# Kernel optimization log

Hardware: AMD Instinct MI355X
Metric: run time of the kernel (lower is better)

The kernel has to match this reference:

```python
import jax, jax.numpy as jnp
import numpy as np

N_MESH, N_GRID, N_EDGES, D, H = 40962, 200000, 600000, 128, 128


def layer_norm(x, g, b, eps=1e-5):
    mu = x.mean(-1, keepdims=True)
    xc = x - mu
    var = (xc * xc).mean(-1, keepdims=True)
    return xc * jax.lax.rsqrt(var + eps) * g + b


def setup_inputs() -> dict:
    key = jax.random.key(0)
    ks = jax.random.split(key, 16)
    s = 1.0 / np.sqrt(D).astype(np.float32)
    s2 = 1.0 / np.sqrt(2 * D).astype(np.float32)
    return {
        "m2g_efeat": jax.random.normal(ks[0], (N_EDGES, D), jnp.float32),
        "grid_nfeat": jax.random.normal(ks[1], (N_GRID, D), jnp.float32),
        "mesh_nfeat": jax.random.normal(ks[2], (N_MESH, D), jnp.float32),
        "src_idx": jax.random.randint(ks[3], (N_EDGES,), 0, N_MESH, jnp.int32),
        "dst_idx": jnp.sort(jax.random.randint(ks[4], (N_EDGES,), 0, N_GRID, jnp.int32)),
        # edge TMLP (first linear split across efeat/src/dst -- equals Linear on concat)
        "We": jax.random.normal(ks[5], (D, H), jnp.float32) * s,
        "Ws": jax.random.normal(ks[6], (D, H), jnp.float32) * s,
        "Wd": jax.random.normal(ks[7], (D, H), jnp.float32) * s,
        "b0": jnp.zeros((H,), jnp.float32),
        "W1e": jax.random.normal(ks[8], (H, D), jnp.float32) * s,
        "b1e": jnp.zeros((D,), jnp.float32),
        "ge": jnp.ones((D,), jnp.float32),
        "be": jnp.zeros((D,), jnp.float32),
        # node MLP: input = concat(grid_nfeat, aggregated_efeat) -> 2D
        "Wn0": jax.random.normal(ks[9], (2 * D, H), jnp.float32) * s2,
        "bn0": jnp.zeros((H,), jnp.float32),
        "Wn1": jax.random.normal(ks[10], (H, D), jnp.float32) * s,
        "bn1": jnp.zeros((D,), jnp.float32),
        "gn": jnp.ones((D,), jnp.float32),
        "bn": jnp.zeros((D,), jnp.float32),
    }


def reference(m2g_efeat, grid_nfeat, mesh_nfeat, src_idx, dst_idx,
              We, Ws, Wd, b0, W1e, b1e, ge, be,
              Wn0, bn0, Wn1, bn1, gn, bn):
    # edge TMLP: project each input tensor then gather (CUGO truncated-MLP form)
    h = jax.nn.silu(m2g_efeat @ We
                    + (mesh_nfeat @ Ws)[src_idx]
                    + (grid_nfeat @ Wd)[dst_idx]
                    + b0)                                  # [E, H]
    efeat = layer_norm(h @ W1e + b1e, ge, be)              # [E, D]
    # sum aggregation edge->node, then concat with dst node features
    agg = jax.ops.segment_sum(efeat, dst_idx, num_segments=grid_nfeat.shape[0])  # [N_grid, D]
    cat = jnp.concatenate([grid_nfeat, agg], axis=-1)      # [N_grid, 2D]
    hn = jax.nn.silu(cat @ Wn0 + bn0)                      # [N_grid, H]
    dst = layer_norm(hn @ Wn1 + bn1, gn, bn) + grid_nfeat  # residual
    return dst
```

## Files before the change

### kernel.cpp

```cpp
#include <hip/hip_runtime.h>
#include <math.h>

#define NM 40962
#define NG 200000
#define NE 600000

typedef unsigned short u16;
typedef unsigned int u32;
typedef __attribute__((ext_vector_type(8))) short short8;
typedef __attribute__((ext_vector_type(4))) float f32x4;

#define OFF_WE 0
#define OFF_WS 16384
#define OFF_WD 32768
#define OFF_W1 49152
#define OFF_W0 65536
#define OFF_WN1 98304
__device__ u16 g_wp[114688];

__device__ __forceinline__ u32 f2bf(float f) {
  u32 u = __float_as_uint(f);
  return (u + 0x7FFFu + ((u >> 16) & 1u)) >> 16;
}
__device__ __forceinline__ float bfl(u32 h) { return __uint_as_float(h << 16); }
__device__ __forceinline__ float bsel(u32 w, int hiHalf) {
  return hiHalf ? __uint_as_float(w & 0xFFFF0000u) : __uint_as_float(w << 16);
}
__device__ __forceinline__ float silu_f(float x) { return x / (1.f + __expf(-x)); }

#define MFMA16(a, b, c) __builtin_amdgcn_mfma_f32_16x16x32_bf16(a, b, c, 0, 0, 0)

__device__ __forceinline__ void pk_hl(const float* __restrict__ f, short8& hi, short8& lo) {
#pragma unroll
  for (int j = 0; j < 8; ++j) {
    u32 h = f2bf(f[j]);
    hi[j] = (short)h;
    lo[j] = (short)f2bf(f[j] - bfl(h));
  }
}

__device__ __forceinline__ void afrag_hl(const float* __restrict__ X, int row, int k0,
                                         short8& hi, short8& lo) {
  const float4* p = (const float4*)(X + (size_t)row * 128 + k0);
  float4 a = p[0], b = p[1];
  float f[8] = {a.x, a.y, a.z, a.w, b.x, b.y, b.z, b.w};
  pk_hl(f, hi, lo);
}

template <int K>
__device__ __forceinline__ short8 bfrag(const u16* __restrict__ Wp, int n, int k0) {
  return *(const short8*)(Wp + (size_t)n * K + k0);
}

__global__ void prep_kernel(const float* __restrict__ W, int off, int kbits, int total) {
  int K = 1 << kbits;
  for (int i = blockIdx.x * blockDim.x + threadIdx.x; i < total;
       i += gridDim.x * blockDim.x) {
    int n = i >> kbits, k = i & (K - 1);
    g_wp[off + i] = (u16)f2bf(W[(size_t)k * 128 + n]);
  }
}

__global__ __launch_bounds__(256) void proj_kernel(const float* __restrict__ X,
                                                   int woff, uint4* __restrict__ O,
                                                   int nrows) {
  const u16* Wp = g_wp + woff;
  const int lane = threadIdx.x & 63, wv = threadIdx.x >> 6;
  const int g = lane >> 4, c = lane & 15;
  const int nw = gridDim.x * 4;
  for (int t = blockIdx.x * 4 + wv; t * 32 < nrows; t += nw) {
    const int n0 = t * 32;
    f32x4 acc[2][8];
#pragma unroll
    for (int mt = 0; mt < 2; ++mt)
#pragma unroll
      for (int nt = 0; nt < 8; ++nt) {
        f32x4 z = {0.f, 0.f, 0.f, 0.f};
        acc[mt][nt] = z;
      }
#pragma unroll
    for (int kt = 0; kt < 4; ++kt) {
      short8 ah[2], al[2];
#pragma unroll
      for (int mt = 0; mt < 2; ++mt) {
        int row = n0 + 16 * mt + c;
        if (row >= nrows) row = nrows - 1;
        afrag_hl(X, row, 32 * kt + 8 * g, ah[mt], al[mt]);
      }
#pragma unroll
      for (int nt = 0; nt < 8; ++nt) {
        short8 b = bfrag<128>(Wp, 16 * nt + c, 32 * kt + 8 * g);
#pragma unroll
        for (int mt = 0; mt < 2; ++mt) {
          acc[mt][nt] = MFMA16(ah[mt], b, acc[mt][nt]);
          acc[mt][nt] = MFMA16(al[mt], b, acc[mt][nt]);
        }
      }
    }
#pragma unroll
    for (int mt = 0; mt < 2; ++mt)
#pragma unroll
      for (int r = 0; r < 4; ++r) {
        int row = n0 + 16 * mt + 4 * g + r;
        if (row < nrows) {
          uint4 v;
          v.x = f2bf(acc[mt][0][r]) | (f2bf(acc[mt][1][r]) << 16);
          v.y = f2bf(acc[mt][2][r]) | (f2bf(acc[mt][3][r]) << 16);
          v.z = f2bf(acc[mt][4][r]) | (f2bf(acc[mt][5][r]) << 16);
          v.w = f2bf(acc[mt][6][r]) | (f2bf(acc[mt][7][r]) << 16);
          O[(size_t)row * 16 + c] = v;
        }
      }
  }
}

__global__ __launch_bounds__(256) void edge_kernel(
    const float* __restrict__ m2g, const uint4* __restrict__ PS,
    const uint4* __restrict__ PD, const int* __restrict__ src_idx,
    const int* __restrict__ dst_idx, const float* __restrict__ b0,
    const float* __restrict__ b1e, const float* __restrict__ ge,
    const float* __restrict__ be, float* __restrict__ agg) {
  const u16* WpE = g_wp + OFF_WE;
  const u16* Wp1 = g_wp + OFF_W1;
  __shared__ __align__(16) u16 hbuf[4][2][32][128];
  const int lane = threadIdx.x & 63, wv = threadIdx.x >> 6;
  const int g = lane >> 4, c = lane & 15;
  float b0p[8], b1p[8], gep[8], bep[8];
#pragma unroll
  for (int nt = 0; nt < 8; ++nt) {
    b0p[nt] = b0[16 * nt + c];
    b1p[nt] = b1e[16 * nt + c];
    gep[nt] = ge[16 * nt + c];
    bep[nt] = be[16 * nt + c];
  }
  const int nw = gridDim.x * 4;
  for (int t = blockIdx.x * 4 + wv; t * 32 < NE; t += nw) {
    const int e0 = t * 32;
    int dd[2][4];
    uint4 ps[2][4], pd[2][4];
#pragma unroll
    for (int mt = 0; mt < 2; ++mt)
#pragma unroll
      for (int r = 0; r < 4; ++r) {
        int e = e0 + 16 * mt + 4 * g + r;
        int s = src_idx[e];
        int d = dst_idx[e];
        dd[mt][r] = d;
        ps[mt][r] = PS[(size_t)s * 16 + c];
        pd[mt][r] = PD[(size_t)d * 16 + c];
      }
    f32x4 acc[2][8];
#pragma unroll
    for (int mt = 0; mt < 2; ++mt)
#pragma unroll
      for (int nt = 0; nt < 8; ++nt) {
        f32x4 a;
#pragma unroll
        for (int r = 0; r < 4; ++r) {
          u32 pw = ((const u32*)&ps[mt][r])[nt >> 1];
          u32 qw = ((const u32*)&pd[mt][r])[nt >> 1];
          a[r] = b0p[nt] + bsel(pw, nt & 1) + bsel(qw, nt & 1);
        }
        acc[mt][nt] = a;
      }
#pragma unroll
    for (int kt = 0; kt < 4; ++kt) {
      short8 ah[2], al[2];
#pragma unroll
      for (int mt = 0; mt < 2; ++mt)
        afrag_hl(m2g, e0 + 16 * mt + c, 32 * kt + 8 * g, ah[mt], al[mt]);
#pragma unroll
      for (int nt = 0; nt < 8; ++nt) {
        short8 b = bfrag<128>(WpE, 16 * nt + c, 32 * kt + 8 * g);
#pragma unroll
        for (int mt = 0; mt < 2; ++mt) {
          acc[mt][nt] = MFMA16(ah[mt], b, acc[mt][nt]);
          acc[mt][nt] = MFMA16(al[mt], b, acc[mt][nt]);
        }
      }
    }
#pragma unroll
    for (int mt = 0; mt < 2; ++mt)
#pragma unroll
      for (int r = 0; r < 4; ++r) {
        int row = 16 * mt + 4 * g + r;
        int sw = (row & 7) << 3;
#pragma unroll
        for (int nt = 0; nt < 8; ++nt) {
          float h = silu_f(acc[mt][nt][r]);
          u32 hb = f2bf(h);
          u32 lb = f2bf(h - bfl(hb));
          int idx = (16 * nt + c) ^ sw;
          hbuf[wv][0][row][idx] = (u16)hb;
          hbuf[wv][1][row][idx] = (u16)lb;
        }
      }
    f32x4 acc2[2][8];
#pragma unroll
    for (int mt = 0; mt < 2; ++mt)
#pragma unroll
      for (int nt = 0; nt < 8; ++nt) {
        f32x4 a = {b1p[nt], b1p[nt], b1p[nt], b1p[nt]};
        acc2[mt][nt] = a;
      }
#pragma unroll
    for (int kt = 0; kt < 4; ++kt) {
      short8 ah[2], al[2];
#pragma unroll
      for (int mt = 0; mt < 2; ++mt) {
        int row = 16 * mt + c;
        int idx = (32 * kt + 8 * g) ^ ((c & 7) << 3);
        ah[mt] = *(const short8*)&hbuf[wv][0][row][idx];
        al[mt] = *(const short8*)&hbuf[wv][1][row][idx];
      }
#pragma unroll
      for (int nt = 0; nt < 8; ++nt) {
        short8 b = bfrag<128>(Wp1, 16 * nt + c, 32 * kt + 8 * g);
#pragma unroll
        for (int mt = 0; mt < 2; ++mt) {
          acc2[mt][nt] = MFMA16(ah[mt], b, acc2[mt][nt]);
          acc2[mt][nt] = MFMA16(al[mt], b, acc2[mt][nt]);
        }
      }
    }
#pragma unroll
    for (int mt = 0; mt < 2; ++mt) {
#pragma unroll
      for (int r = 0; r < 4; ++r) {
        float sm = 0.f, sq = 0.f;
#pragma unroll
        for (int nt = 0; nt < 8; ++nt) {
          float v = acc2[mt][nt][r];
          sm += v;
          sq += v * v;
        }
#pragma unroll
        for (int m = 1; m < 16; m <<= 1) {
          sm += __shfl_xor(sm, m, 64);
          sq += __shfl_xor(sq, m, 64);
        }
        float mu = sm * (1.f / 128.f);
        float var = sq * (1.f / 128.f) - mu * mu;
        float rs = rsqrtf(var + 1e-5f);
#pragma unroll
        for (int nt = 0; nt < 8; ++nt)
          acc2[mt][nt][r] = (acc2[mt][nt][r] - mu) * rs * gep[nt] + bep[nt];
      }
#pragma unroll
      for (int nt = 0; nt < 8; ++nt) {
        float a = acc2[mt][nt][0];
        int dp = dd[mt][0];
#pragma unroll
        for (int r = 1; r < 4; ++r) {
          if (dd[mt][r] == dp) {
            a += acc2[mt][nt][r];
          } else {
            atomicAdd(agg + (size_t)dp * 128 + 16 * nt + c, a);
            a = acc2[mt][nt][r];
            dp = dd[mt][r];
          }
        }
        atomicAdd(agg + (size_t)dp * 128 + 16 * nt + c, a);
      }
    }
  }
}

__global__ __launch_bounds__(256) void node_kernel(
    const float* __restrict__ gridf, const float* __restrict__ agg,
    const float* __restrict__ bn0, const float* __restrict__ bn1,
    const float* __restrict__ gn, const float* __restrict__ bnv,
    float* __restrict__ out) {
  const u16* Wp0 = g_wp + OFF_W0;
  const u16* Wp1 = g_wp + OFF_WN1;
  __shared__ __align__(16) u16 hbuf[4][32][128];
  const int lane = threadIdx.x & 63, wv = threadIdx.x >> 6;
  const int g = lane >> 4, c = lane & 15;
  float b0p[8], b1p[8], gp[8], bp[8];
#pragma unroll
  for (int nt = 0; nt < 8; ++nt) {
    b0p[nt] = bn0[16 * nt + c];
    b1p[nt] = bn1[16 * nt + c];
    gp[nt] = gn[16 * nt + c];
    bp[nt] = bnv[16 * nt + c];
  }
  const int nw = gridDim.x * 4;
  for (int t = blockIdx.x * 4 + wv; t * 32 < NG; t += nw) {
    const int n0 = t * 32;
    f32x4 acc[2][8];
#pragma unroll
    for (int mt = 0; mt < 2; ++mt)
#pragma unroll
      for (int nt = 0; nt < 8; ++nt) {
        f32x4 a = {b0p[nt], b0p[nt], b0p[nt], b0p[nt]};
        acc[mt][nt] = a;
      }
#pragma unroll
    for (int kt = 0; kt < 8; ++kt) {
      const float* src = (kt < 4) ? gridf : agg;
      int k0 = (kt & 3) * 32 + 8 * g;
      short8 ah[2], al[2];
#pragma unroll
      for (int mt = 0; mt < 2; ++mt) afrag_hl(src, n0 + 16 * mt + c, k0, ah[mt], al[mt]);
#pragma unroll
      for (int nt = 0; nt < 8; ++nt) {
        short8 b = bfrag<256>(Wp0, 16 * nt + c, 32 * kt + 8 * g);
#pragma unroll
        for (int mt = 0; mt < 2; ++mt) {
          acc[mt][nt] = MFMA16(ah[mt], b, acc[mt][nt]);
          acc[mt][nt] = MFMA16(al[mt], b, acc[mt][nt]);
        }
      }
    }
#pragma unroll
    for (int mt = 0; mt < 2; ++mt)
#pragma unroll
      for (int r = 0; r < 4; ++r) {
        int row = 16 * mt + 4 * g + r;
        int sw = (row & 7) << 3;
#pragma unroll
        for (int nt = 0; nt < 8; ++nt)
          hbuf[wv][row][(16 * nt + c) ^ sw] = (u16)f2bf(silu_f(acc[mt][nt][r]));
      }
    f32x4 acc2[2][8];
#pragma unroll
    for (int mt = 0; mt < 2; ++mt)
#pragma unroll
      for (int nt = 0; nt < 8; ++nt) {
        f32x4 a = {b1p[nt], b1p[nt], b1p[nt], b1p[nt]};
        acc2[mt][nt] = a;
      }
#pragma unroll
    for (int kt = 0; kt < 4; ++kt) {
      short8 ah[2];
#pragma unroll
      for (int mt = 0; mt < 2; ++mt) {
        int row = 16 * mt + c;
        ah[mt] = *(const short8*)&hbuf[wv][row][(32 * kt + 8 * g) ^ ((c & 7) << 3)];
      }
#pragma unroll
      for (int nt = 0; nt < 8; ++nt) {
        short8 b = bfrag<128>(Wp1, 16 * nt + c, 32 * kt + 8 * g);
#pragma unroll
        for (int mt = 0; mt < 2; ++mt) acc2[mt][nt] = MFMA16(ah[mt], b, acc2[mt][nt]);
      }
    }
#pragma unroll
    for (int mt = 0; mt < 2; ++mt)
#pragma unroll
      for (int r = 0; r < 4; ++r) {
        float sm = 0.f, sq = 0.f;
#pragma unroll
        for (int nt = 0; nt < 8; ++nt) {
          float v = acc2[mt][nt][r];
          sm += v;
          sq += v * v;
        }
#pragma unroll
        for (int m = 1; m < 16; m <<= 1) {
          sm += __shfl_xor(sm, m, 64);
          sq += __shfl_xor(sq, m, 64);
        }
        float mu = sm * (1.f / 128.f);
        float var = sq * (1.f / 128.f) - mu * mu;
        float rs = rsqrtf(var + 1e-5f);
        int row = n0 + 16 * mt + 4 * g + r;
#pragma unroll
        for (int nt = 0; nt < 8; ++nt) {
          size_t o = (size_t)row * 128 + 16 * nt + c;
          out[o] = (acc2[mt][nt][r] - mu) * rs * gp[nt] + bp[nt] + gridf[o];
        }
      }
  }
}

extern "C" void kernel_launch(void* const* d_in, const int* in_sizes, int n_in,
                              void* d_out, int out_size, void* d_ws, size_t ws_size,
                              hipStream_t stream) {
  const float* m2g = (const float*)d_in[0];
  const float* grid = (const float*)d_in[1];
  const float* mesh = (const float*)d_in[2];
  const int* src = (const int*)d_in[3];
  const int* dst = (const int*)d_in[4];
  const float* We = (const float*)d_in[5];
  const float* Ws = (const float*)d_in[6];
  const float* Wd = (const float*)d_in[7];
  const float* b0 = (const float*)d_in[8];
  const float* W1e = (const float*)d_in[9];
  const float* b1e = (const float*)d_in[10];
  const float* ge = (const float*)d_in[11];
  const float* be = (const float*)d_in[12];
  const float* Wn0 = (const float*)d_in[13];
  const float* bn0 = (const float*)d_in[14];
  const float* Wn1 = (const float*)d_in[15];
  const float* bn1 = (const float*)d_in[16];
  const float* gn = (const float*)d_in[17];
  const float* bnv = (const float*)d_in[18];
  (void)in_sizes; (void)n_in; (void)out_size; (void)ws_size;

  char* ws = (char*)d_ws;
  float* agg = (float*)ws;
  size_t aggB = (size_t)NG * 128 * 4;
  size_t psB = (size_t)NM * 256;
  uint4* PS = (uint4*)(ws + aggB);
  uint4* PD = (uint4*)(ws + aggB + psB);

  prep_kernel<<<64, 256, 0, stream>>>(We, OFF_WE, 7, 16384);
  prep_kernel<<<64, 256, 0, stream>>>(Ws, OFF_WS, 7, 16384);
  prep_kernel<<<64, 256, 0, stream>>>(Wd, OFF_WD, 7, 16384);
  prep_kernel<<<64, 256, 0, stream>>>(W1e, OFF_W1, 7, 16384);
  prep_kernel<<<128, 256, 0, stream>>>(Wn0, OFF_W0, 8, 32768);
  prep_kernel<<<64, 256, 0, stream>>>(Wn1, OFF_WN1, 7, 16384);
  hipMemsetAsync(agg, 0, aggB, stream);
  proj_kernel<<<512, 256, 0, stream>>>(mesh, OFF_WS, PS, NM);
  proj_kernel<<<512, 256, 0, stream>>>(grid, OFF_WD, PD, NG);
  edge_kernel<<<512, 256, 0, stream>>>(m2g, PS, PD, src, dst, b0, b1e, ge, be, agg);
  node_kernel<<<512, 256, 0, stream>>>(grid, agg, bn0, bn1, gn, bnv, (float*)d_out);
}
```

Baseline: 1.230 ms.

## Merge weight prep and projection launches, fold agg zeroing, prefetch edge inputs

```diff
diff --git a/kernel.cpp b/kernel.cpp
--- a/kernel.cpp
+++ b/kernel.cpp
@@ -30,7 +30,9 @@
 
 #define MFMA16(a, b, c) __builtin_amdgcn_mfma_f32_16x16x32_bf16(a, b, c, 0, 0, 0)
 
-__device__ __forceinline__ void pk_hl(const float* __restrict__ f, short8& hi, short8& lo) {
+__device__ __forceinline__ void pk8(const float4& a, const float4& b, short8& hi,
+                                    short8& lo) {
+  float f[8] = {a.x, a.y, a.z, a.w, b.x, b.y, b.z, b.w};
 #pragma unroll
   for (int j = 0; j < 8; ++j) {
     u32 h = f2bf(f[j]);
@@ -42,9 +44,7 @@
 __device__ __forceinline__ void afrag_hl(const float* __restrict__ X, int row, int k0,
                                          short8& hi, short8& lo) {
   const float4* p = (const float4*)(X + (size_t)row * 128 + k0);
-  float4 a = p[0], b = p[1];
-  float f[8] = {a.x, a.y, a.z, a.w, b.x, b.y, b.z, b.w};
-  pk_hl(f, hi, lo);
+  pk8(p[0], p[1], hi, lo);
 }
 
 template <int K>
@@ -52,24 +52,41 @@
   return *(const short8*)(Wp + (size_t)n * K + k0);
 }
 
-__global__ void prep_kernel(const float* __restrict__ W, int off, int kbits, int total) {
-  int K = 1 << kbits;
-  for (int i = blockIdx.x * blockDim.x + threadIdx.x; i < total;
+__global__ void prep_all(const float* __restrict__ We, const float* __restrict__ Ws,
+                         const float* __restrict__ Wd, const float* __restrict__ W1e,
+                         const float* __restrict__ Wn0, const float* __restrict__ Wn1) {
+  for (int i = blockIdx.x * blockDim.x + threadIdx.x; i < 114688;
        i += gridDim.x * blockDim.x) {
-    int n = i >> kbits, k = i & (K - 1);
-    g_wp[off + i] = (u16)f2bf(W[(size_t)k * 128 + n]);
-  }
-}
-
-__global__ __launch_bounds__(256) void proj_kernel(const float* __restrict__ X,
-                                                   int woff, uint4* __restrict__ O,
-                                                   int nrows) {
-  const u16* Wp = g_wp + woff;
+    const float* W;
+    int loc, kb;
+    if (i < 16384)       { W = We;  loc = i;         kb = 7; }
+    else if (i < 32768)  { W = Ws;  loc = i - 16384; kb = 7; }
+    else if (i < 49152)  { W = Wd;  loc = i - 32768; kb = 7; }
+    else if (i < 65536)  { W = W1e; loc = i - 49152; kb = 7; }
+    else if (i < 98304)  { W = Wn0; loc = i - 65536; kb = 8; }
+    else                 { W = Wn1; loc = i - 98304; kb = 7; }
+    int n = loc >> kb, k = loc & ((1 << kb) - 1);
+    g_wp[i] = (u16)f2bf(W[(size_t)k * 128 + n]);
+  }
+}
+
+__global__ __launch_bounds__(256) void proj_kernel(const float* __restrict__ mesh,
+                                                   const float* __restrict__ gridf,
+                                                   uint4* __restrict__ PS,
+                                                   uint4* __restrict__ PD,
+                                                   float* __restrict__ agg) {
+  const int TM = (NM + 31) / 32;
+  const int TG = NG / 32;
   const int lane = threadIdx.x & 63, wv = threadIdx.x >> 6;
   const int g = lane >> 4, c = lane & 15;
   const int nw = gridDim.x * 4;
-  for (int t = blockIdx.x * 4 + wv; t * 32 < nrows; t += nw) {
-    const int n0 = t * 32;
+  for (int t = blockIdx.x * 4 + wv; t < TM + TG; t += nw) {
+    const float* X;
+    const u16* Wp;
+    uint4* O;
+    int n0, nrows, zero;
+    if (t < TM) { X = mesh;  Wp = g_wp + OFF_WS; O = PS; n0 = t * 32;        nrows = NM; zero = 0; }
+    else        { X = gridf; Wp = g_wp + OFF_WD; O = PD; n0 = (t - TM) * 32; nrows = NG; zero = 1; }
     f32x4 acc[2][8];
 #pragma unroll
     for (int mt = 0; mt < 2; ++mt)
@@ -109,6 +126,12 @@
           v.z = f2bf(acc[mt][4][r]) | (f2bf(acc[mt][5][r]) << 16);
           v.w = f2bf(acc[mt][6][r]) | (f2bf(acc[mt][7][r]) << 16);
           O[(size_t)row * 16 + c] = v;
+          if (zero) {
+            float4 z = {0.f, 0.f, 0.f, 0.f};
+            float4* ap = (float4*)(agg + (size_t)row * 128 + c * 8);
+            ap[0] = z;
+            ap[1] = z;
+          }
         }
       }
   }
@@ -122,20 +145,26 @@
     const float* __restrict__ be, float* __restrict__ agg) {
   const u16* WpE = g_wp + OFF_WE;
   const u16* Wp1 = g_wp + OFF_W1;
-  __shared__ __align__(16) u16 hbuf[4][2][32][128];
+  __shared__ __align__(16) u16 hbh[4][32][128];
+  __shared__ __align__(16) u16 hbl[4][32][128];
   const int lane = threadIdx.x & 63, wv = threadIdx.x >> 6;
   const int g = lane >> 4, c = lane & 15;
-  float b0p[8], b1p[8], gep[8], bep[8];
-#pragma unroll
-  for (int nt = 0; nt < 8; ++nt) {
-    b0p[nt] = b0[16 * nt + c];
-    b1p[nt] = b1e[16 * nt + c];
-    gep[nt] = ge[16 * nt + c];
-    bep[nt] = be[16 * nt + c];
-  }
+  float b0p[8];
+#pragma unroll
+  for (int nt = 0; nt < 8; ++nt) b0p[nt] = b0[16 * nt + c];
   const int nw = gridDim.x * 4;
-  for (int t = blockIdx.x * 4 + wv; t * 32 < NE; t += nw) {
+  for (int t = blockIdx.x * 4 + wv; t < NE / 32; t += nw) {
     const int e0 = t * 32;
+    float4 av[2][4][2];
+#pragma unroll
+    for (int mt = 0; mt < 2; ++mt)
+#pragma unroll
+      for (int kt = 0; kt < 4; ++kt) {
+        const float4* p =
+            (const float4*)(m2g + (size_t)(e0 + 16 * mt + c) * 128 + 32 * kt + 8 * g);
+        av[mt][kt][0] = p[0];
+        av[mt][kt][1] = p[1];
+      }
     int dd[2][4];
     uint4 ps[2][4], pd[2][4];
 #pragma unroll
@@ -154,31 +183,34 @@
     for (int mt = 0; mt < 2; ++mt)
 #pragma unroll
       for (int nt = 0; nt < 8; ++nt) {
-        f32x4 a;
+        f32x4 z = {0.f, 0.f, 0.f, 0.f};
+        acc[mt][nt] = z;
+      }
+#pragma unroll
+    for (int kt = 0; kt < 4; ++kt) {
+      short8 ah[2], al[2];
+#pragma unroll
+      for (int mt = 0; mt < 2; ++mt) pk8(av[mt][kt][0], av[mt][kt][1], ah[mt], al[mt]);
+#pragma unroll
+      for (int nt = 0; nt < 8; ++nt) {
+        short8 b = bfrag<128>(WpE, 16 * nt + c, 32 * kt + 8 * g);
+#pragma unroll
+        for (int mt = 0; mt < 2; ++mt) {
+          acc[mt][nt] = MFMA16(ah[mt], b, acc[mt][nt]);
+          acc[mt][nt] = MFMA16(al[mt], b, acc[mt][nt]);
+        }
+      }
+    }
+#pragma unroll
+    for (int mt = 0; mt < 2; ++mt)
+#pragma unroll
+      for (int nt = 0; nt < 8; ++nt)
 #pragma unroll
         for (int r = 0; r < 4; ++r) {
           u32 pw = ((const u32*)&ps[mt][r])[nt >> 1];
           u32 qw = ((const u32*)&pd[mt][r])[nt >> 1];
-          a[r] = b0p[nt] + bsel(pw, nt & 1) + bsel(qw, nt & 1);
-        }
-        acc[mt][nt] = a;
-      }
-#pragma unroll
-    for (int kt = 0; kt < 4; ++kt) {
-      short8 ah[2], al[2];
-#pragma unroll
-      for (int mt = 0; mt < 2; ++mt)
-        afrag_hl(m2g, e0 + 16 * mt + c, 32 * kt + 8 * g, ah[mt], al[mt]);
-#pragma unroll
-      for (int nt = 0; nt < 8; ++nt) {
-        short8 b = bfrag<128>(WpE, 16 * nt + c, 32 * kt + 8 * g);
-#pragma unroll
-        for (int mt = 0; mt < 2; ++mt) {
-          acc[mt][nt] = MFMA16(ah[mt], b, acc[mt][nt]);
-          acc[mt][nt] = MFMA16(al[mt], b, acc[mt][nt]);
-        }
-      }
-    }
+          acc[mt][nt][r] += b0p[nt] + bsel(pw, nt & 1) + bsel(qw, nt & 1);
+        }
 #pragma unroll
     for (int mt = 0; mt < 2; ++mt)
 #pragma unroll
@@ -191,18 +223,23 @@
           u32 hb = f2bf(h);
           u32 lb = f2bf(h - bfl(hb));
           int idx = (16 * nt + c) ^ sw;
-          hbuf[wv][0][row][idx] = (u16)hb;
-          hbuf[wv][1][row][idx] = (u16)lb;
+          hbh[wv][row][idx] = (u16)hb;
+          hbl[wv][row][idx] = (u16)lb;
         }
       }
     f32x4 acc2[2][8];
-#pragma unroll
-    for (int mt = 0; mt < 2; ++mt)
-#pragma unroll
-      for (int nt = 0; nt < 8; ++nt) {
-        f32x4 a = {b1p[nt], b1p[nt], b1p[nt], b1p[nt]};
-        acc2[mt][nt] = a;
-      }
+    {
+      float b1p[8];
+#pragma unroll
+      for (int nt = 0; nt < 8; ++nt) b1p[nt] = b1e[16 * nt + c];
+#pragma unroll
+      for (int mt = 0; mt < 2; ++mt)
+#pragma unroll
+        for (int nt = 0; nt < 8; ++nt) {
+          f32x4 a = {b1p[nt], b1p[nt], b1p[nt], b1p[nt]};
+          acc2[mt][nt] = a;
+        }
+    }
 #pragma unroll
     for (int kt = 0; kt < 4; ++kt) {
       short8 ah[2], al[2];
@@ -210,8 +247,8 @@
       for (int mt = 0; mt < 2; ++mt) {
         int row = 16 * mt + c;
         int idx = (32 * kt + 8 * g) ^ ((c & 7) << 3);
-        ah[mt] = *(const short8*)&hbuf[wv][0][row][idx];
-        al[mt] = *(const short8*)&hbuf[wv][1][row][idx];
+        ah[mt] = *(const short8*)&hbh[wv][row][idx];
+        al[mt] = *(const short8*)&hbl[wv][row][idx];
       }
 #pragma unroll
       for (int nt = 0; nt < 8; ++nt) {
@@ -222,6 +259,12 @@
           acc2[mt][nt] = MFMA16(al[mt], b, acc2[mt][nt]);
         }
       }
+    }
+    float gep[8], bep[8];
+#pragma unroll
+    for (int nt = 0; nt < 8; ++nt) {
+      gep[nt] = ge[16 * nt + c];
+      bep[nt] = be[16 * nt + c];
     }
 #pragma unroll
     for (int mt = 0; mt < 2; ++mt) {
@@ -273,19 +316,17 @@
     float* __restrict__ out) {
   const u16* Wp0 = g_wp + OFF_W0;
   const u16* Wp1 = g_wp + OFF_WN1;
-  __shared__ __align__(16) u16 hbuf[4][32][128];
+  __shared__ __align__(16) u16 nbuf[4][32][128];
   const int lane = threadIdx.x & 63, wv = threadIdx.x >> 6;
   const int g = lane >> 4, c = lane & 15;
-  float b0p[8], b1p[8], gp[8], bp[8];
+  float b0p[8], b1p[8];
 #pragma unroll
   for (int nt = 0; nt < 8; ++nt) {
     b0p[nt] = bn0[16 * nt + c];
     b1p[nt] = bn1[16 * nt + c];
-    gp[nt] = gn[16 * nt + c];
-    bp[nt] = bnv[16 * nt + c];
   }
   const int nw = gridDim.x * 4;
-  for (int t = blockIdx.x * 4 + wv; t * 32 < NG; t += nw) {
+  for (int t = blockIdx.x * 4 + wv; t < NG / 32; t += nw) {
     const int n0 = t * 32;
     f32x4 acc[2][8];
 #pragma unroll
@@ -320,7 +361,7 @@
         int sw = (row & 7) << 3;
 #pragma unroll
         for (int nt = 0; nt < 8; ++nt)
-          hbuf[wv][row][(16 * nt + c) ^ sw] = (u16)f2bf(silu_f(acc[mt][nt][r]));
+          nbuf[wv][row][(16 * nt + c) ^ sw] = (u16)f2bf(silu_f(acc[mt][nt][r]));
       }
     f32x4 acc2[2][8];
 #pragma unroll
@@ -336,7 +377,7 @@
 #pragma unroll
       for (int mt = 0; mt < 2; ++mt) {
         int row = 16 * mt + c;
-        ah[mt] = *(const short8*)&hbuf[wv][row][(32 * kt + 8 * g) ^ ((c & 7) << 3)];
+        ah[mt] = *(const short8*)&nbuf[wv][row][(32 * kt + 8 * g) ^ ((c & 7) << 3)];
       }
 #pragma unroll
       for (int nt = 0; nt < 8; ++nt) {
@@ -344,6 +385,12 @@
 #pragma unroll
         for (int mt = 0; mt < 2; ++mt) acc2[mt][nt] = MFMA16(ah[mt], b, acc2[mt][nt]);
       }
+    }
+    float gp[8], bp[8];
+#pragma unroll
+    for (int nt = 0; nt < 8; ++nt) {
+      gp[nt] = gn[16 * nt + c];
+      bp[nt] = bnv[16 * nt + c];
     }
 #pragma unroll
     for (int mt = 0; mt < 2; ++mt)
@@ -405,15 +452,8 @@
   uint4* PS = (uint4*)(ws + aggB);
   uint4* PD = (uint4*)(ws + aggB + psB);
 
-  prep_kernel<<<64, 256, 0, stream>>>(We, OFF_WE, 7, 16384);
-  prep_kernel<<<64, 256, 0, stream>>>(Ws, OFF_WS, 7, 16384);
-  prep_kernel<<<64, 256, 0, stream>>>(Wd, OFF_WD, 7, 16384);
-  prep_kernel<<<64, 256, 0, stream>>>(W1e, OFF_W1, 7, 16384);
-  prep_kernel<<<128, 256, 0, stream>>>(Wn0, OFF_W0, 8, 32768);
-  prep_kernel<<<64, 256, 0, stream>>>(Wn1, OFF_WN1, 7, 16384);
-  hipMemsetAsync(agg, 0, aggB, stream);
-  proj_kernel<<<512, 256, 0, stream>>>(mesh, OFF_WS, PS, NM);
-  proj_kernel<<<512, 256, 0, stream>>>(grid, OFF_WD, PD, NG);
-  edge_kernel<<<512, 256, 0, stream>>>(m2g, PS, PD, src, dst, b0, b1e, ge, be, agg);
-  node_kernel<<<512, 256, 0, stream>>>(grid, agg, bn0, bn1, gn, bnv, (float*)d_out);
-}
+  prep_all<<<224, 256, 0, stream>>>(We, Ws, Wd, W1e, Wn0, Wn1);
+  proj_kernel<<<1024, 256, 0, stream>>>(mesh, grid, PS, PD, agg);
+  edge_kernel<<<1536, 256, 0, stream>>>(m2g, PS, PD, src, dst, b0, b1e, ge, be, agg);
+  node_kernel<<<1536, 256, 0, stream>>>(grid, agg, bn0, bn1, gn, bnv, (float*)d_out);
+}
```

New measurement: 1.210 ms. Within noise of the previous version (-1.7%).
